# Optimization experiments

Hardware: AMD Instinct MI355X
Metric: run time of the kernel (lower is better)

The kernel has to match this reference:

```python
import jax, jax.numpy as jnp
import numpy as np

C = 8.0


def _linear_scan(alpha, xbeta):
    # h_t = alpha_t * h_{t-1} + xbeta_t, scan over time axis=1
    def combine(e1, e2):
        a1, b1 = e1
        a2, b2 = e2
        return a2 * a1, a2 * b1 + b2
    _, h = jax.lax.associative_scan(combine, (alpha, xbeta), axis=1)
    return h


def setup_inputs() -> dict:
    dim = 2048
    B, T = 4, 4096
    key = jax.random.key(0)
    k_x, k_wi, k_wg = jax.random.split(key, 3)
    std = dim ** -0.5
    x = jax.random.normal(k_x, (B, T, dim), dtype=jnp.float32)
    W_in = jax.random.normal(k_wi, (dim, dim), dtype=jnp.float32) * std
    b_in = jnp.zeros((dim,), dtype=jnp.float32)
    W_gate = jax.random.normal(k_wg, (dim, dim), dtype=jnp.float32) * std
    b_gate = jnp.zeros((dim,), dtype=jnp.float32)
    forget_lambda = jnp.linspace(-4.323, -9.0, dim, dtype=jnp.float32)
    return {"x": x, "W_in": W_in, "b_in": b_in, "W_gate": W_gate,
            "b_gate": b_gate, "forget_lambda": forget_lambda}


def reference(x, W_in, b_in, W_gate, b_gate, forget_lambda):
    # x: [B, T, D]
    input_gate = jnp.einsum('btd,ed->bte', x, W_in) + b_in
    recurrence_gate = jnp.einsum('btd,ed->bte', x, W_gate) + b_gate
    # alpha_t = exp(-C * softplus(lambda) * sigmoid(r_t))  per channel
    alpha = jnp.exp(-C * jax.nn.softplus(forget_lambda) * jax.nn.sigmoid(recurrence_gate))
    beta = jnp.sqrt(1.0 - alpha ** 2 + 1e-6)
    xbeta = beta * jax.nn.sigmoid(input_gate) * x
    return _linear_scan(alpha, xbeta)
```

## Files before the change

### kernel.cpp

```cpp
#include <hip/hip_runtime.h>

typedef unsigned short u16;
typedef unsigned int u32;

using bf16x8 = __attribute__((ext_vector_type(8))) __bf16;
using f32x4  = __attribute__((ext_vector_type(4))) float;
using u16x8  = __attribute__((ext_vector_type(8))) u16;

#define BB 4
#define TT 4096
#define DD 2048
#define MM 16384
#define KK 2048
#define NCHUNK 16
#define CLEN 256

__device__ __forceinline__ u16 f2bf(float f) {
    u32 u = __float_as_uint(f);
    u32 r = (u + 0x7FFFu + ((u >> 16) & 1u)) >> 16;
    return (u16)r;
}

__device__ __forceinline__ void gload_lds16(const void* g, void* l) {
    __builtin_amdgcn_global_load_lds(
        (const __attribute__((address_space(1))) void*)g,
        (__attribute__((address_space(3))) void*)l, 16, 0, 0);
}

#define BAR() do { __builtin_amdgcn_sched_barrier(0); __builtin_amdgcn_s_barrier(); __builtin_amdgcn_sched_barrier(0); } while(0)
#define WAIT_LGKM0() do { asm volatile("s_waitcnt lgkmcnt(0)" ::: "memory"); __builtin_amdgcn_sched_barrier(0); } while(0)
#define WAIT_VM8() do { asm volatile("s_waitcnt vmcnt(8)" ::: "memory"); __builtin_amdgcn_sched_barrier(0); } while(0)
#define WAIT_VM4() do { asm volatile("s_waitcnt vmcnt(4)" ::: "memory"); __builtin_amdgcn_sched_barrier(0); } while(0)
#define WAIT_VM0() do { asm volatile("s_waitcnt vmcnt(0)" ::: "memory"); __builtin_amdgcn_sched_barrier(0); } while(0)

__global__ __launch_bounds__(256) void cvt_kernel(const float* __restrict__ in,
                                                  u16* __restrict__ out, int n8) {
    int i = blockIdx.x * 256 + threadIdx.x;
    if (i >= n8) return;
    const f32x4* p = (const f32x4*)in + (size_t)i * 2;
    f32x4 a = p[0], b = p[1];
    u16x8 o;
    o[0] = f2bf(a[0]); o[1] = f2bf(a[1]); o[2] = f2bf(a[2]); o[3] = f2bf(a[3]);
    o[4] = f2bf(b[0]); o[5] = f2bf(b[1]); o[6] = f2bf(b[2]); o[7] = f2bf(b[3]);
    *((u16x8*)out + i) = o;
}

#define BMg 256
#define BNg 128
#define BKg 32
#define NT (KK / BKg)

__global__ __launch_bounds__(512, 2) void gemm_dual8(
    const u16* __restrict__ xb, const u16* __restrict__ wib, const u16* __restrict__ wgb,
    const float* __restrict__ xf,
    const float* __restrict__ b_in, const float* __restrict__ b_gate,
    const float* __restrict__ lam, u32* __restrict__ pair)
{
    __shared__ u16 As[4][BMg * BKg];
    __shared__ u16 Bs[4][2][BNg * BKg];

    const int tid = threadIdx.x;
    const int bid = blockIdx.x;
    const int cpx = gridDim.x >> 3;
    const int swz = (bid & 7) * cpx + (bid >> 3);
    const int et = swz & 15;
    const int mt = swz >> 4;
    const size_t m0 = (size_t)mt * BMg;
    const size_t e0 = (size_t)et * BNg;

    const int lane = tid & 63;
    const int wid = tid >> 6;
    const int wr = wid >> 2;
    const int wc = wid & 3;
    const int r15 = lane & 15;
    const int s4 = lane >> 4;

    const int srow = tid >> 2;
    const int sseg = (tid & 3) ^ ((tid >> 3) & 3);
    const int skp  = sseg << 3;

    const int koff = ((s4 ^ ((r15 >> 1) & 3)) << 3);

#define STAGE_A(t) do { int _b = (t) & 3; size_t _k = (size_t)(t) * BKg + skp; \
        gload_lds16(xb + (m0 + srow) * KK + _k,        &As[_b][tid * 8]); \
        gload_lds16(xb + (m0 + 128 + srow) * KK + _k,  &As[_b][4096 + tid * 8]); } while (0)
#define STAGE_B(t) do { int _b = (t) & 3; size_t _k = (size_t)(t) * BKg + skp; \
        gload_lds16(wib + (e0 + srow) * KK + _k, &Bs[_b][0][tid * 8]); \
        gload_lds16(wgb + (e0 + srow) * KK + _k, &Bs[_b][1][tid * 8]); } while (0)

    f32x4 accI[8][2], accG[8][2];
#pragma unroll
    for (int i = 0; i < 8; i++)
#pragma unroll
        for (int j = 0; j < 2; j++) {
            accI[i][j] = (f32x4){0.f, 0.f, 0.f, 0.f};
            accG[i][j] = (f32x4){0.f, 0.f, 0.f, 0.f};
        }

    STAGE_A(0); STAGE_B(0);
    STAGE_A(1); STAGE_B(1);
    STAGE_A(2); STAGE_B(2);
    WAIT_VM8();
    BAR();

    for (int t = 0; t < NT; ++t) {
        const int cb = t & 3;
        const u16* Ab = &As[cb][0];
        const u16* BiB = &Bs[cb][0][0];
        const u16* BgB = &Bs[cb][1][0];
        bf16x8 bI[2], bG[2], aF[4];

#pragma unroll
        for (int q = 0; q < 4; q++)
            aF[q] = *(const bf16x8*)&Ab[(wr * 128 + q * 16 + r15) * BKg + koff];
#pragma unroll
        for (int ni = 0; ni < 2; ni++) {
            bI[ni] = *(const bf16x8*)&BiB[(wc * 32 + ni * 16 + r15) * BKg + koff];
            bG[ni] = *(const bf16x8*)&BgB[(wc * 32 + ni * 16 + r15) * BKg + koff];
        }
        if (t < NT - 3) STAGE_A(t + 3);
        BAR();
        WAIT_LGKM0();
        __builtin_amdgcn_s_setprio(1);
#pragma unroll
        for (int q = 0; q < 4; q++)
#pragma unroll
            for (int ni = 0; ni < 2; ni++) {
                accI[q][ni] = __builtin_amdgcn_mfma_f32_16x16x32_bf16(aF[q], bI[ni], accI[q][ni], 0, 0, 0);
                accG[q][ni] = __builtin_amdgcn_mfma_f32_16x16x32_bf16(aF[q], bG[ni], accG[q][ni], 0, 0, 0);
            }
        __builtin_amdgcn_s_setprio(0);
        BAR();

#pragma unroll
        for (int q = 0; q < 4; q++)
            aF[q] = *(const bf16x8*)&Ab[(wr * 128 + (q + 4) * 16 + r15) * BKg + koff];
        if (t < NT - 3) STAGE_B(t + 3);
        BAR();
        WAIT_LGKM0();
        __builtin_amdgcn_s_setprio(1);
#pragma unroll
        for (int q = 0; q < 4; q++)
#pragma unroll
            for (int ni = 0; ni < 2; ni++) {
                accI[q + 4][ni] = __builtin_amdgcn_mfma_f32_16x16x32_bf16(aF[q], bI[ni], accI[q + 4][ni], 0, 0, 0);
                accG[q + 4][ni] = __builtin_amdgcn_mfma_f32_16x16x32_bf16(aF[q], bG[ni], accG[q + 4][ni], 0, 0, 0);
            }
        __builtin_amdgcn_s_setprio(0);
        if (t < NT - 3)      WAIT_VM8();
        else if (t == NT - 3) WAIT_VM4();
        else                  WAIT_VM0();
        BAR();
    }

    float spl[2], biv[2], bgv[2];
    size_t ecol[2];
#pragma unroll
    for (int ni = 0; ni < 2; ni++) {
        size_t e = e0 + wc * 32 + ni * 16 + r15;
        ecol[ni] = e;
        spl[ni] = 8.0f * log1pf(__expf(lam[e]));
        biv[ni] = b_in[e];
        bgv[ni] = b_gate[e];
    }
    const int rbase = s4 * 4;
#pragma unroll
    for (int mi = 0; mi < 8; mi++) {
#pragma unroll
        for (int r = 0; r < 4; r++) {
            size_t m = m0 + wr * 128 + mi * 16 + rbase + r;
#pragma unroll
            for (int ni = 0; ni < 2; ni++) {
                size_t e = ecol[ni];
                float ig = accI[mi][ni][r] + biv[ni];
                float rg = accG[mi][ni][r] + bgv[ni];
                float sigr = 1.f / (1.f + __expf(-rg));
                float g = spl[ni] * sigr;
                float beta = sqrtf(1.f - __expf(-2.f * g) + 1e-6f);
                float xv = xf[m * DD + e];
                float xbeta = beta * (1.f / (1.f + __expf(-ig))) * xv;
                u32 pk = (u32)f2bf(g) | (((u32)f2bf(xbeta)) << 16);
                pair[m * DD + e] = pk;
            }
        }
    }
#undef STAGE_A
#undef STAGE_B
}

__global__ __launch_bounds__(256) void scanA(const u32* __restrict__ pair,
                                             float* __restrict__ aggG,
                                             float* __restrict__ aggB) {
    int gid = blockIdx.x * 256 + threadIdx.x;
    int e = gid & (DD - 1);
    int rest = gid >> 11;
    int b = rest & 3;
    int c = rest >> 2;
    const u32* p = pair + ((size_t)(b * TT + c * CLEN)) * DD + e;
    float gsum = 0.f, h = 0.f;
#pragma unroll 4
    for (int t = 0; t < CLEN; ++t) {
        u32 v = *p; p += DD;
        float gf = __uint_as_float(v << 16);
        float xbv = __uint_as_float(v & 0xFFFF0000u);
        gsum += gf;
        h = fmaf(__expf(-gf), h, xbv);
    }
    int idx = ((b * NCHUNK + c) << 11) | e;
    aggG[idx] = gsum;
    aggB[idx] = h;
}

__global__ __launch_bounds__(256) void scanB(const float* __restrict__ aggG,
                                             const float* __restrict__ aggB,
                                             float* __restrict__ carry) {
    int gid = blockIdx.x * 256 + threadIdx.x;
    int e = gid & (DD - 1);
    int b = gid >> 11;
    float h = 0.f;
#pragma unroll
    for (int c = 0; c < NCHUNK; ++c) {
        int idx = ((b * NCHUNK + c) << 11) | e;
        carry[idx] = h;
        h = fmaf(__expf(-aggG[idx]), h, aggB[idx]);
    }
}

__global__ __launch_bounds__(256) void scanC(const u32* __restrict__ pair,
                                             const float* __restrict__ carry,
                                             float* __restrict__ out) {
    int gid = blockIdx.x * 256 + threadIdx.x;
    int e = gid & (DD - 1);
    int rest = gid >> 11;
    int b = rest & 3;
    int c = rest >> 2;
    const u32* p = pair + ((size_t)(b * TT + c * CLEN)) * DD + e;
    float* o = out + ((size_t)(b * TT + c * CLEN)) * DD + e;
    float h = carry[((b * NCHUNK + c) << 11) | e];
#pragma unroll 4
    for (int t = 0; t < CLEN; ++t) {
        u32 v = *p; p += DD;
        float gf = __uint_as_float(v << 16);
        float xbv = __uint_as_float(v & 0xFFFF0000u);
        h = fmaf(__expf(-gf), h, xbv);
        *o = h; o += DD;
    }
}

extern "C" void kernel_launch(void* const* d_in, const int* in_sizes, int n_in,
                              void* d_out, int out_size, void* d_ws, size_t ws_size,
                              hipStream_t stream) {
    const float* x      = (const float*)d_in[0];
    const float* W_in   = (const float*)d_in[1];
    const float* b_in   = (const float*)d_in[2];
    const float* W_gate = (const float*)d_in[3];
    const float* b_gate = (const float*)d_in[4];
    const float* lam    = (const float*)d_in[5];
    float* out = (float*)d_out;

    char* ws = (char*)d_ws;
    u16* xb   = (u16*)(ws);
    u16* wib  = (u16*)(ws + 67108864);
    u16* wgb  = (u16*)(ws + 75497472);
    u32* pair = (u32*)(ws + 83886080);
    float* aggG  = (float*)(ws + 218103808);
    float* aggB  = (float*)(ws + 218628096);
    float* carry = (float*)(ws + 219152384);

    cvt_kernel<<<16384, 256, 0, stream>>>(x, xb, MM * KK / 8);
    cvt_kernel<<<2048, 256, 0, stream>>>(W_in, wib, DD * KK / 8);
    cvt_kernel<<<2048, 256, 0, stream>>>(W_gate, wgb, DD * KK / 8);
    gemm_dual8<<<(MM / BMg) * (DD / BNg), 512, 0, stream>>>(xb, wib, wgb, x, b_in, b_gate, lam, pair);
    scanA<<<BB * DD * NCHUNK / 256, 256, 0, stream>>>(pair, aggG, aggB);
    scanB<<<BB * DD / 256, 256, 0, stream>>>(aggG, aggB, carry);
    scanC<<<BB * DD * NCHUNK / 256, 256, 0, stream>>>(pair, carry, out);
}
```

Measured before the change: 503.5 us.

## Restructure GEMM main loop with hoisted offsets and read bf16 x in epilogue

The GEMM K-loop is split into a steady-state loop unrolled by 4 without staging branches and a separate tail loop. LDS fragment offsets and global base pointers are precomputed once instead of per iteration. The sched_barrier wrappers around the barriers are removed, giving the compiler more scheduling freedom. The epilogue reads x from the bf16 copy instead of the fp32 input, halving that traffic but lowering the precision of x in xbeta.

Result: faster. 436.3 us (-13.3%).

```diff
diff --git a/kernel.cpp b/kernel.cpp
--- a/kernel.cpp
+++ b/kernel.cpp
@@ -26,12 +26,6 @@
         (const __attribute__((address_space(1))) void*)g,
         (__attribute__((address_space(3))) void*)l, 16, 0, 0);
 }
-
-#define BAR() do { __builtin_amdgcn_sched_barrier(0); __builtin_amdgcn_s_barrier(); __builtin_amdgcn_sched_barrier(0); } while(0)
-#define WAIT_LGKM0() do { asm volatile("s_waitcnt lgkmcnt(0)" ::: "memory"); __builtin_amdgcn_sched_barrier(0); } while(0)
-#define WAIT_VM8() do { asm volatile("s_waitcnt vmcnt(8)" ::: "memory"); __builtin_amdgcn_sched_barrier(0); } while(0)
-#define WAIT_VM4() do { asm volatile("s_waitcnt vmcnt(4)" ::: "memory"); __builtin_amdgcn_sched_barrier(0); } while(0)
-#define WAIT_VM0() do { asm volatile("s_waitcnt vmcnt(0)" ::: "memory"); __builtin_amdgcn_sched_barrier(0); } while(0)
 
 __global__ __launch_bounds__(256) void cvt_kernel(const float* __restrict__ in,
                                                   u16* __restrict__ out, int n8) {
@@ -52,7 +46,6 @@
 
 __global__ __launch_bounds__(512, 2) void gemm_dual8(
     const u16* __restrict__ xb, const u16* __restrict__ wib, const u16* __restrict__ wgb,
-    const float* __restrict__ xf,
     const float* __restrict__ b_in, const float* __restrict__ b_gate,
     const float* __restrict__ lam, u32* __restrict__ pair)
 {
@@ -81,12 +74,23 @@
 
     const int koff = ((s4 ^ ((r15 >> 1) & 3)) << 3);
 
-#define STAGE_A(t) do { int _b = (t) & 3; size_t _k = (size_t)(t) * BKg + skp; \
-        gload_lds16(xb + (m0 + srow) * KK + _k,        &As[_b][tid * 8]); \
-        gload_lds16(xb + (m0 + 128 + srow) * KK + _k,  &As[_b][4096 + tid * 8]); } while (0)
-#define STAGE_B(t) do { int _b = (t) & 3; size_t _k = (size_t)(t) * BKg + skp; \
-        gload_lds16(wib + (e0 + srow) * KK + _k, &Bs[_b][0][tid * 8]); \
-        gload_lds16(wgb + (e0 + srow) * KK + _k, &Bs[_b][1][tid * 8]); } while (0)
+    const u16* gA0 = xb  + (m0 + srow) * KK + skp;
+    const u16* gA1 = gA0 + (size_t)128 * KK;
+    const u16* gI  = wib + (e0 + srow) * KK + skp;
+    const u16* gG  = wgb + (e0 + srow) * KK + skp;
+
+    int aoff[8], boff[2];
+#pragma unroll
+    for (int q = 0; q < 8; q++) aoff[q] = (wr * 128 + q * 16 + r15) * BKg + koff;
+#pragma unroll
+    for (int ni = 0; ni < 2; ni++) boff[ni] = (wc * 32 + ni * 16 + r15) * BKg + koff;
+
+#define STAGE_A(t) do { int _b = (t) & 3; size_t _k = (size_t)(t) * BKg; \
+        gload_lds16(gA0 + _k, &As[_b][tid * 8]); \
+        gload_lds16(gA1 + _k, &As[_b][4096 + tid * 8]); } while (0)
+#define STAGE_B(t) do { int _b = (t) & 3; size_t _k = (size_t)(t) * BKg; \
+        gload_lds16(gI + _k, &Bs[_b][0][tid * 8]); \
+        gload_lds16(gG + _k, &Bs[_b][1][tid * 8]); } while (0)
 
     f32x4 accI[8][2], accG[8][2];
 #pragma unroll
@@ -100,57 +104,61 @@
     STAGE_A(0); STAGE_B(0);
     STAGE_A(1); STAGE_B(1);
     STAGE_A(2); STAGE_B(2);
-    WAIT_VM8();
-    BAR();
-
-    for (int t = 0; t < NT; ++t) {
-        const int cb = t & 3;
-        const u16* Ab = &As[cb][0];
-        const u16* BiB = &Bs[cb][0][0];
-        const u16* BgB = &Bs[cb][1][0];
-        bf16x8 bI[2], bG[2], aF[4];
-
-#pragma unroll
-        for (int q = 0; q < 4; q++)
-            aF[q] = *(const bf16x8*)&Ab[(wr * 128 + q * 16 + r15) * BKg + koff];
-#pragma unroll
-        for (int ni = 0; ni < 2; ni++) {
-            bI[ni] = *(const bf16x8*)&BiB[(wc * 32 + ni * 16 + r15) * BKg + koff];
-            bG[ni] = *(const bf16x8*)&BgB[(wc * 32 + ni * 16 + r15) * BKg + koff];
-        }
-        if (t < NT - 3) STAGE_A(t + 3);
-        BAR();
-        WAIT_LGKM0();
-        __builtin_amdgcn_s_setprio(1);
-#pragma unroll
-        for (int q = 0; q < 4; q++)
-#pragma unroll
-            for (int ni = 0; ni < 2; ni++) {
-                accI[q][ni] = __builtin_amdgcn_mfma_f32_16x16x32_bf16(aF[q], bI[ni], accI[q][ni], 0, 0, 0);
-                accG[q][ni] = __builtin_amdgcn_mfma_f32_16x16x32_bf16(aF[q], bG[ni], accG[q][ni], 0, 0, 0);
-            }
-        __builtin_amdgcn_s_setprio(0);
-        BAR();
-
-#pragma unroll
-        for (int q = 0; q < 4; q++)
-            aF[q] = *(const bf16x8*)&Ab[(wr * 128 + (q + 4) * 16 + r15) * BKg + koff];
-        if (t < NT - 3) STAGE_B(t + 3);
-        BAR();
-        WAIT_LGKM0();
-        __builtin_amdgcn_s_setprio(1);
-#pragma unroll
-        for (int q = 0; q < 4; q++)
-#pragma unroll
-            for (int ni = 0; ni < 2; ni++) {
-                accI[q + 4][ni] = __builtin_amdgcn_mfma_f32_16x16x32_bf16(aF[q], bI[ni], accI[q + 4][ni], 0, 0, 0);
-                accG[q + 4][ni] = __builtin_amdgcn_mfma_f32_16x16x32_bf16(aF[q], bG[ni], accG[q + 4][ni], 0, 0, 0);
-            }
-        __builtin_amdgcn_s_setprio(0);
-        if (t < NT - 3)      WAIT_VM8();
-        else if (t == NT - 3) WAIT_VM4();
-        else                  WAIT_VM0();
-        BAR();
+    asm volatile("s_waitcnt vmcnt(8)" ::: "memory");
+    __builtin_amdgcn_s_barrier();
+
+#define PHASE0(t) do { \
+        const u16* Ab = &As[(t) & 3][0]; \
+        const u16* BiB = &Bs[(t) & 3][0][0]; \
+        const u16* BgB = &Bs[(t) & 3][1][0]; \
+        _Pragma("unroll") for (int q = 0; q < 4; q++) aF[q] = *(const bf16x8*)&Ab[aoff[q]]; \
+        _Pragma("unroll") for (int ni = 0; ni < 2; ni++) { \
+            bI[ni] = *(const bf16x8*)&BiB[boff[ni]]; \
+            bG[ni] = *(const bf16x8*)&BgB[boff[ni]]; } \
+    } while (0)
+#define PHASE1(t) do { \
+        const u16* Ab = &As[(t) & 3][0]; \
+        _Pragma("unroll") for (int q = 0; q < 4; q++) aF[q] = *(const bf16x8*)&Ab[aoff[q + 4]]; \
+    } while (0)
+#define MFMA_BURST(base) do { \
+        asm volatile("s_waitcnt lgkmcnt(0)" ::: "memory"); \
+        __builtin_amdgcn_sched_barrier(0); \
+        __builtin_amdgcn_s_setprio(1); \
+        _Pragma("unroll") for (int q = 0; q < 4; q++) \
+        _Pragma("unroll") for (int ni = 0; ni < 2; ni++) { \
+            accI[q + (base)][ni] = __builtin_amdgcn_mfma_f32_16x16x32_bf16(aF[q], bI[ni], accI[q + (base)][ni], 0, 0, 0); \
+            accG[q + (base)][ni] = __builtin_amdgcn_mfma_f32_16x16x32_bf16(aF[q], bG[ni], accG[q + (base)][ni], 0, 0, 0); } \
+        __builtin_amdgcn_s_setprio(0); \
+    } while (0)
+
+    bf16x8 bI[2], bG[2], aF[4];
+
+#pragma unroll 4
+    for (int t = 0; t < NT - 3; ++t) {
+        PHASE0(t);
+        STAGE_A(t + 3);
+        __builtin_amdgcn_s_barrier();
+        MFMA_BURST(0);
+        __builtin_amdgcn_s_barrier();
+        PHASE1(t);
+        STAGE_B(t + 3);
+        __builtin_amdgcn_s_barrier();
+        MFMA_BURST(4);
+        asm volatile("s_waitcnt vmcnt(8)" ::: "memory");
+        __builtin_amdgcn_s_barrier();
+    }
+#pragma unroll 1
+    for (int t = NT - 3; t < NT; ++t) {
+        PHASE0(t);
+        __builtin_amdgcn_s_barrier();
+        MFMA_BURST(0);
+        __builtin_amdgcn_s_barrier();
+        PHASE1(t);
+        __builtin_amdgcn_s_barrier();
+        MFMA_BURST(4);
+        if (t == NT - 3) asm volatile("s_waitcnt vmcnt(4)" ::: "memory");
+        else             asm volatile("s_waitcnt vmcnt(0)" ::: "memory");
+        __builtin_amdgcn_s_barrier();
     }
 
     float spl[2], biv[2], bgv[2];
@@ -177,7 +185,7 @@
                 float sigr = 1.f / (1.f + __expf(-rg));
                 float g = spl[ni] * sigr;
                 float beta = sqrtf(1.f - __expf(-2.f * g) + 1e-6f);
-                float xv = xf[m * DD + e];
+                float xv = __uint_as_float((u32)xb[m * KK + e] << 16);
                 float xbeta = beta * (1.f / (1.f + __expf(-ig))) * xv;
                 u32 pk = (u32)f2bf(g) | (((u32)f2bf(xbeta)) << 16);
                 pair[m * DD + e] = pk;
@@ -186,6 +194,9 @@
     }
 #undef STAGE_A
 #undef STAGE_B
+#undef PHASE0
+#undef PHASE1
+#undef MFMA_BURST
 }
 
 __global__ __launch_bounds__(256) void scanA(const u32* __restrict__ pair,
@@ -270,7 +281,7 @@
     cvt_kernel<<<16384, 256, 0, stream>>>(x, xb, MM * KK / 8);
     cvt_kernel<<<2048, 256, 0, stream>>>(W_in, wib, DD * KK / 8);
     cvt_kernel<<<2048, 256, 0, stream>>>(W_gate, wgb, DD * KK / 8);
-    gemm_dual8<<<(MM / BMg) * (DD / BNg), 512, 0, stream>>>(xb, wib, wgb, x, b_in, b_gate, lam, pair);
+    gemm_dual8<<<(MM / BMg) * (DD / BNg), 512, 0, stream>>>(xb, wib, wgb, b_in, b_gate, lam, pair);
     scanA<<<BB * DD * NCHUNK / 256, 256, 0, stream>>>(pair, aggG, aggB);
     scanB<<<BB * DD / 256, 256, 0, stream>>>(aggG, aggB, carry);
     scanC<<<BB * DD * NCHUNK / 256, 256, 0, stream>>>(pair, carry, out);
```

## Restructure dual GEMM into double-buffered BK=64 pipeline with register-prefetched fragments

Applied to the files above, without the earlier changes.

Rewrites the main loop of the dual GEMM to use a 64-wide K tile with two LDS buffers and an XOR-swizzled layout. LDS fragment reads for the next MFMA burst are interleaved with the current burst, and the global-to-LDS loads are split into four sub-stages placed between bursts. The aim is to hide LDS and global latency behind MFMA work. The epilogue now reads x from the bf16 copy instead of the fp32 input, which halves that read traffic but uses a rounded x value in xbeta. LDS use stays the same while register pressure rises because of the prefetched fragments.

After: 571.5 us. 13.5% more time.

```diff
diff --git a/kernel.cpp b/kernel.cpp
--- a/kernel.cpp
+++ b/kernel.cpp
@@ -26,12 +26,6 @@
         (const __attribute__((address_space(1))) void*)g,
         (__attribute__((address_space(3))) void*)l, 16, 0, 0);
 }
-
-#define BAR() do { __builtin_amdgcn_sched_barrier(0); __builtin_amdgcn_s_barrier(); __builtin_amdgcn_sched_barrier(0); } while(0)
-#define WAIT_LGKM0() do { asm volatile("s_waitcnt lgkmcnt(0)" ::: "memory"); __builtin_amdgcn_sched_barrier(0); } while(0)
-#define WAIT_VM8() do { asm volatile("s_waitcnt vmcnt(8)" ::: "memory"); __builtin_amdgcn_sched_barrier(0); } while(0)
-#define WAIT_VM4() do { asm volatile("s_waitcnt vmcnt(4)" ::: "memory"); __builtin_amdgcn_sched_barrier(0); } while(0)
-#define WAIT_VM0() do { asm volatile("s_waitcnt vmcnt(0)" ::: "memory"); __builtin_amdgcn_sched_barrier(0); } while(0)
 
 __global__ __launch_bounds__(256) void cvt_kernel(const float* __restrict__ in,
                                                   u16* __restrict__ out, int n8) {
@@ -47,17 +41,19 @@
 
 #define BMg 256
 #define BNg 128
-#define BKg 32
-#define NT (KK / BKg)
-
-__global__ __launch_bounds__(512, 2) void gemm_dual8(
+#define BKt 64
+#define NTt (KK / BKt)
+
+#define MF(a_, b_, c_) __builtin_amdgcn_mfma_f32_16x16x32_bf16(a_, b_, c_, 0, 0, 0)
+
+__global__ __launch_bounds__(512, 2) void gemm_dual_p4(
     const u16* __restrict__ xb, const u16* __restrict__ wib, const u16* __restrict__ wgb,
-    const float* __restrict__ xf,
     const float* __restrict__ b_in, const float* __restrict__ b_gate,
     const float* __restrict__ lam, u32* __restrict__ pair)
 {
-    __shared__ u16 As[4][BMg * BKg];
-    __shared__ u16 Bs[4][2][BNg * BKg];
+    __shared__ u16 As[2][BMg * BKt];
+    __shared__ u16 Bi[2][BNg * BKt];
+    __shared__ u16 Bg[2][BNg * BKt];
 
     const int tid = threadIdx.x;
     const int bid = blockIdx.x;
@@ -69,24 +65,50 @@
     const size_t e0 = (size_t)et * BNg;
 
     const int lane = tid & 63;
-    const int wid = tid >> 6;
-    const int wr = wid >> 2;
-    const int wc = wid & 3;
+    const int w = tid >> 6;
+    const int wr = w >> 2;
+    const int wc = w & 3;
     const int r15 = lane & 15;
     const int s4 = lane >> 4;
 
-    const int srow = tid >> 2;
-    const int sseg = (tid & 3) ^ ((tid >> 3) & 3);
-    const int skp  = sseg << 3;
-
-    const int koff = ((s4 ^ ((r15 >> 1) & 3)) << 3);
-
-#define STAGE_A(t) do { int _b = (t) & 3; size_t _k = (size_t)(t) * BKg + skp; \
-        gload_lds16(xb + (m0 + srow) * KK + _k,        &As[_b][tid * 8]); \
-        gload_lds16(xb + (m0 + 128 + srow) * KK + _k,  &As[_b][4096 + tid * 8]); } while (0)
-#define STAGE_B(t) do { int _b = (t) & 3; size_t _k = (size_t)(t) * BKg + skp; \
-        gload_lds16(wib + (e0 + srow) * KK + _k, &Bs[_b][0][tid * 8]); \
-        gload_lds16(wgb + (e0 + srow) * KK + _k, &Bs[_b][1][tid * 8]); } while (0)
+    const u16 *gSA0[2], *gSA1[2], *gSBI[2], *gSBG[2];
+#pragma unroll
+    for (int j = 0; j < 2; j++) {
+        int L = w * 128 + j * 64 + lane;
+        int row = L >> 3;
+        int sc = (L & 7) ^ (row & 7);
+        gSA0[j] = xb  + (m0 + row) * (size_t)KK + sc * 8;
+        gSA1[j] = xb  + (m0 + 128 + row) * (size_t)KK + sc * 8;
+        gSBI[j] = wib + (e0 + row) * (size_t)KK + sc * 8;
+        gSBG[j] = wgb + (e0 + row) * (size_t)KK + sc * 8;
+    }
+    const int dstE = (w * 128 + lane) * 8;
+
+#define ST_A0(t) do { int _b = ((t) & 1); size_t _k = (size_t)(t) * BKt; \
+        gload_lds16(gSA0[0] + _k, &As[_b][dstE]); \
+        gload_lds16(gSA0[1] + _k, &As[_b][dstE + 512]); } while (0)
+#define ST_A1(t) do { int _b = ((t) & 1); size_t _k = (size_t)(t) * BKt; \
+        gload_lds16(gSA1[0] + _k, &As[_b][8192 + dstE]); \
+        gload_lds16(gSA1[1] + _k, &As[_b][8192 + dstE + 512]); } while (0)
+#define ST_BI(t) do { int _b = ((t) & 1); size_t _k = (size_t)(t) * BKt; \
+        gload_lds16(gSBI[0] + _k, &Bi[_b][dstE]); \
+        gload_lds16(gSBI[1] + _k, &Bi[_b][dstE + 512]); } while (0)
+#define ST_BG(t) do { int _b = ((t) & 1); size_t _k = (size_t)(t) * BKt; \
+        gload_lds16(gSBG[0] + _k, &Bg[_b][dstE]); \
+        gload_lds16(gSBG[1] + _k, &Bg[_b][dstE + 512]); } while (0)
+
+    int cE[2];
+#pragma unroll
+    for (int ks = 0; ks < 2; ks++) cE[ks] = ((((ks << 2) | s4) ^ (r15 & 7)) << 3);
+    int aR[8], bR[2];
+#pragma unroll
+    for (int mF = 0; mF < 8; mF++) aR[mF] = (wr * 128 + mF * 16 + r15) << 6;
+#pragma unroll
+    for (int ni = 0; ni < 2; ni++) bR[ni] = (wc * 32 + ni * 16 + r15) << 6;
+
+#define RD_A(b_, mF_, ks_)  (*(const bf16x8*)&As[b_][aR[mF_] + cE[ks_]])
+#define RD_BI(b_, ni_, ks_) (*(const bf16x8*)&Bi[b_][bR[ni_] + cE[ks_]])
+#define RD_BG(b_, ni_, ks_) (*(const bf16x8*)&Bg[b_][bR[ni_] + cE[ks_]])
 
     f32x4 accI[8][2], accG[8][2];
 #pragma unroll
@@ -97,60 +119,120 @@
             accG[i][j] = (f32x4){0.f, 0.f, 0.f, 0.f};
         }
 
-    STAGE_A(0); STAGE_B(0);
-    STAGE_A(1); STAGE_B(1);
-    STAGE_A(2); STAGE_B(2);
-    WAIT_VM8();
-    BAR();
-
-    for (int t = 0; t < NT; ++t) {
-        const int cb = t & 3;
-        const u16* Ab = &As[cb][0];
-        const u16* BiB = &Bs[cb][0][0];
-        const u16* BgB = &Bs[cb][1][0];
-        bf16x8 bI[2], bG[2], aF[4];
-
-#pragma unroll
-        for (int q = 0; q < 4; q++)
-            aF[q] = *(const bf16x8*)&Ab[(wr * 128 + q * 16 + r15) * BKg + koff];
-#pragma unroll
-        for (int ni = 0; ni < 2; ni++) {
-            bI[ni] = *(const bf16x8*)&BiB[(wc * 32 + ni * 16 + r15) * BKg + koff];
-            bG[ni] = *(const bf16x8*)&BgB[(wc * 32 + ni * 16 + r15) * BKg + koff];
-        }
-        if (t < NT - 3) STAGE_A(t + 3);
-        BAR();
-        WAIT_LGKM0();
-        __builtin_amdgcn_s_setprio(1);
-#pragma unroll
-        for (int q = 0; q < 4; q++)
-#pragma unroll
-            for (int ni = 0; ni < 2; ni++) {
-                accI[q][ni] = __builtin_amdgcn_mfma_f32_16x16x32_bf16(aF[q], bI[ni], accI[q][ni], 0, 0, 0);
-                accG[q][ni] = __builtin_amdgcn_mfma_f32_16x16x32_bf16(aF[q], bG[ni], accG[q][ni], 0, 0, 0);
-            }
-        __builtin_amdgcn_s_setprio(0);
-        BAR();
-
-#pragma unroll
-        for (int q = 0; q < 4; q++)
-            aF[q] = *(const bf16x8*)&Ab[(wr * 128 + (q + 4) * 16 + r15) * BKg + koff];
-        if (t < NT - 3) STAGE_B(t + 3);
-        BAR();
-        WAIT_LGKM0();
-        __builtin_amdgcn_s_setprio(1);
-#pragma unroll
-        for (int q = 0; q < 4; q++)
-#pragma unroll
-            for (int ni = 0; ni < 2; ni++) {
-                accI[q + 4][ni] = __builtin_amdgcn_mfma_f32_16x16x32_bf16(aF[q], bI[ni], accI[q + 4][ni], 0, 0, 0);
-                accG[q + 4][ni] = __builtin_amdgcn_mfma_f32_16x16x32_bf16(aF[q], bG[ni], accG[q + 4][ni], 0, 0, 0);
-            }
-        __builtin_amdgcn_s_setprio(0);
-        if (t < NT - 3)      WAIT_VM8();
-        else if (t == NT - 3) WAIT_VM4();
-        else                  WAIT_VM0();
-        BAR();
+    bf16x8 aA[4], aB[4], aC[4], aD[4];
+    bf16x8 b0v[4], b1v[4];
+
+#define LGKM(n) do { asm volatile("s_waitcnt lgkmcnt(" #n ")" ::: "memory"); \
+                     __builtin_amdgcn_sched_barrier(0); } while (0)
+#define VMC(n)  asm volatile("s_waitcnt vmcnt(" #n ")" ::: "memory")
+#define BARx()  __builtin_amdgcn_s_barrier()
+#define BURST(aV, bV, base) do { __builtin_amdgcn_s_setprio(1); \
+        _Pragma("unroll") for (int m = 0; m < 4; m++) { \
+            accI[m + (base)][0] = MF(aV[m], bV[0], accI[m + (base)][0]); \
+            accI[m + (base)][1] = MF(aV[m], bV[1], accI[m + (base)][1]); \
+            accG[m + (base)][0] = MF(aV[m], bV[2], accG[m + (base)][0]); \
+            accG[m + (base)][1] = MF(aV[m], bV[3], accG[m + (base)][1]); } \
+        __builtin_amdgcn_s_setprio(0); } while (0)
+
+    ST_A0(0); ST_A1(0); ST_BI(0); ST_BG(0);
+    ST_A0(1); ST_A1(1); ST_BI(1); ST_BG(1);
+    VMC(8);
+    BARx();
+
+    {
+#pragma unroll
+        for (int m = 0; m < 4; m++) aA[m] = RD_A(0, m, 0);
+#pragma unroll
+        for (int n = 0; n < 2; n++) { b0v[n] = RD_BI(0, n, 0); b0v[2 + n] = RD_BG(0, n, 0); }
+#pragma unroll
+        for (int m = 0; m < 4; m++) aB[m] = RD_A(0, m + 4, 0);
+#pragma unroll
+        for (int m = 0; m < 4; m++) aC[m] = RD_A(0, m, 1);
+#pragma unroll
+        for (int n = 0; n < 2; n++) { b1v[n] = RD_BI(0, n, 1); b1v[2 + n] = RD_BG(0, n, 1); }
+        BARx();
+        LGKM(8);
+        BURST(aA, b0v, 0);
+#pragma unroll
+        for (int m = 0; m < 4; m++) aD[m] = RD_A(0, m + 4, 1);
+        BARx();
+        LGKM(4);
+        BURST(aB, b0v, 4);
+        VMC(4);
+        BARx();
+    }
+
+#pragma unroll 2
+    for (int t = 1; t < NTt - 1; ++t) {
+        const int b = t & 1;
+#pragma unroll
+        for (int m = 0; m < 4; m++) aA[m] = RD_A(b, m, 0);
+        ST_A0(t + 1);
+        BARx();
+        LGKM(4);
+        BURST(aC, b1v, 0);
+        VMC(2);
+        BARx();
+#pragma unroll
+        for (int n = 0; n < 2; n++) { b0v[n] = RD_BI(b, n, 0); b0v[2 + n] = RD_BG(b, n, 0); }
+#pragma unroll
+        for (int m = 0; m < 4; m++) aB[m] = RD_A(b, m + 4, 0);
+        ST_A1(t + 1);
+        BARx();
+        LGKM(8);
+        BURST(aD, b1v, 4);
+        BARx();
+#pragma unroll
+        for (int m = 0; m < 4; m++) aC[m] = RD_A(b, m, 1);
+#pragma unroll
+        for (int n = 0; n < 2; n++) { b1v[n] = RD_BI(b, n, 1); b1v[2 + n] = RD_BG(b, n, 1); }
+        ST_BI(t + 1);
+        BARx();
+        LGKM(8);
+        BURST(aA, b0v, 0);
+        BARx();
+#pragma unroll
+        for (int m = 0; m < 4; m++) aD[m] = RD_A(b, m + 4, 1);
+        ST_BG(t + 1);
+        BARx();
+        LGKM(4);
+        BURST(aB, b0v, 4);
+        VMC(4);
+        BARx();
+    }
+
+    {
+#pragma unroll
+        for (int m = 0; m < 4; m++) aA[m] = RD_A(1, m, 0);
+        BARx();
+        LGKM(4);
+        BURST(aC, b1v, 0);
+        VMC(0);
+        BARx();
+#pragma unroll
+        for (int n = 0; n < 2; n++) { b0v[n] = RD_BI(1, n, 0); b0v[2 + n] = RD_BG(1, n, 0); }
+#pragma unroll
+        for (int m = 0; m < 4; m++) aB[m] = RD_A(1, m + 4, 0);
+        BARx();
+        LGKM(8);
+        BURST(aD, b1v, 4);
+        BARx();
+#pragma unroll
+        for (int m = 0; m < 4; m++) aC[m] = RD_A(1, m, 1);
+#pragma unroll
+        for (int n = 0; n < 2; n++) { b1v[n] = RD_BI(1, n, 1); b1v[2 + n] = RD_BG(1, n, 1); }
+        BARx();
+        LGKM(8);
+        BURST(aA, b0v, 0);
+        BARx();
+#pragma unroll
+        for (int m = 0; m < 4; m++) aD[m] = RD_A(1, m + 4, 1);
+        BARx();
+        LGKM(4);
+        BURST(aB, b0v, 4);
+        LGKM(0);
+        BURST(aC, b1v, 0);
+        BURST(aD, b1v, 4);
     }
 
     float spl[2], biv[2], bgv[2];
@@ -177,15 +259,21 @@
                 float sigr = 1.f / (1.f + __expf(-rg));
                 float g = spl[ni] * sigr;
                 float beta = sqrtf(1.f - __expf(-2.f * g) + 1e-6f);
-                float xv = xf[m * DD + e];
+                float xv = __uint_as_float((u32)xb[m * KK + e] << 16);
                 float xbeta = beta * (1.f / (1.f + __expf(-ig))) * xv;
                 u32 pk = (u32)f2bf(g) | (((u32)f2bf(xbeta)) << 16);
                 pair[m * DD + e] = pk;
             }
         }
     }
-#undef STAGE_A
-#undef STAGE_B
+#undef ST_A0
+#undef ST_A1
+#undef ST_BI
+#undef ST_BG
+#undef RD_A
+#undef RD_BI
+#undef RD_BG
+#undef BURST
 }
 
 __global__ __launch_bounds__(256) void scanA(const u32* __restrict__ pair,
@@ -270,7 +358,7 @@
     cvt_kernel<<<16384, 256, 0, stream>>>(x, xb, MM * KK / 8);
     cvt_kernel<<<2048, 256, 0, stream>>>(W_in, wib, DD * KK / 8);
     cvt_kernel<<<2048, 256, 0, stream>>>(W_gate, wgb, DD * KK / 8);
-    gemm_dual8<<<(MM / BMg) * (DD / BNg), 512, 0, stream>>>(xb, wib, wgb, x, b_in, b_gate, lam, pair);
+    gemm_dual_p4<<<(MM / BMg) * (DD / BNg), 512, 0, stream>>>(xb, wib, wgb, b_in, b_gate, lam, pair);
     scanA<<<BB * DD * NCHUNK / 256, 256, 0, stream>>>(pair, aggG, aggB);
     scanB<<<BB * DD / 256, 256, 0, stream>>>(aggG, aggB, carry);
     scanC<<<BB * DD * NCHUNK / 256, 256, 0, stream>>>(pair, carry, out);
```

## Rework dual GEMM pipeline: prefetch depth two, new LDS swizzle, bf16 x in epilogue

Applied to the files above, without the earlier changes.

Restructures the dual-GEMM main loop. Prefetch distance drops from three stages to two with adjusted vmcnt waits, and the sched_barrier wrappers around barriers are removed. Global pointers and LDS offsets are precomputed with a new XOR swizzle intended to reduce bank conflicts. The epilogue reads x from the bf16 copy instead of fp32 to cut global traffic, at some precision cost in xbeta. A shallower prefetch may expose more load latency.

Result: faster. 472.8 us (-6.1%).

```diff
diff --git a/kernel.cpp b/kernel.cpp
--- a/kernel.cpp
+++ b/kernel.cpp
@@ -26,12 +26,6 @@
         (const __attribute__((address_space(1))) void*)g,
         (__attribute__((address_space(3))) void*)l, 16, 0, 0);
 }
-
-#define BAR() do { __builtin_amdgcn_sched_barrier(0); __builtin_amdgcn_s_barrier(); __builtin_amdgcn_sched_barrier(0); } while(0)
-#define WAIT_LGKM0() do { asm volatile("s_waitcnt lgkmcnt(0)" ::: "memory"); __builtin_amdgcn_sched_barrier(0); } while(0)
-#define WAIT_VM8() do { asm volatile("s_waitcnt vmcnt(8)" ::: "memory"); __builtin_amdgcn_sched_barrier(0); } while(0)
-#define WAIT_VM4() do { asm volatile("s_waitcnt vmcnt(4)" ::: "memory"); __builtin_amdgcn_sched_barrier(0); } while(0)
-#define WAIT_VM0() do { asm volatile("s_waitcnt vmcnt(0)" ::: "memory"); __builtin_amdgcn_sched_barrier(0); } while(0)
 
 __global__ __launch_bounds__(256) void cvt_kernel(const float* __restrict__ in,
                                                   u16* __restrict__ out, int n8) {
@@ -50,14 +44,16 @@
 #define BKg 32
 #define NT (KK / BKg)
 
-__global__ __launch_bounds__(512, 2) void gemm_dual8(
+#define MF(a_, b_, c_) __builtin_amdgcn_mfma_f32_16x16x32_bf16(a_, b_, c_, 0, 0, 0)
+
+__global__ __launch_bounds__(512, 2) void gemm_lock2(
     const u16* __restrict__ xb, const u16* __restrict__ wib, const u16* __restrict__ wgb,
-    const float* __restrict__ xf,
     const float* __restrict__ b_in, const float* __restrict__ b_gate,
     const float* __restrict__ lam, u32* __restrict__ pair)
 {
     __shared__ u16 As[4][BMg * BKg];
-    __shared__ u16 Bs[4][2][BNg * BKg];
+    __shared__ u16 Bi[4][BNg * BKg];
+    __shared__ u16 Bg[4][BNg * BKg];
 
     const int tid = threadIdx.x;
     const int bid = blockIdx.x;
@@ -69,24 +65,40 @@
     const size_t e0 = (size_t)et * BNg;
 
     const int lane = tid & 63;
-    const int wid = tid >> 6;
-    const int wr = wid >> 2;
-    const int wc = wid & 3;
+    const int w = tid >> 6;
+    const int wr = w >> 2;
+    const int wc = w & 3;
     const int r15 = lane & 15;
     const int s4 = lane >> 4;
 
-    const int srow = tid >> 2;
-    const int sseg = (tid & 3) ^ ((tid >> 3) & 3);
-    const int skp  = sseg << 3;
-
-    const int koff = ((s4 ^ ((r15 >> 1) & 3)) << 3);
-
-#define STAGE_A(t) do { int _b = (t) & 3; size_t _k = (size_t)(t) * BKg + skp; \
-        gload_lds16(xb + (m0 + srow) * KK + _k,        &As[_b][tid * 8]); \
-        gload_lds16(xb + (m0 + 128 + srow) * KK + _k,  &As[_b][4096 + tid * 8]); } while (0)
-#define STAGE_B(t) do { int _b = (t) & 3; size_t _k = (size_t)(t) * BKg + skp; \
-        gload_lds16(wib + (e0 + srow) * KK + _k, &Bs[_b][0][tid * 8]); \
-        gload_lds16(wgb + (e0 + srow) * KK + _k, &Bs[_b][1][tid * 8]); } while (0)
+    const u16 *gA[2], *gBi, *gBg;
+#pragma unroll
+    for (int j = 0; j < 2; j++) {
+        int L = j * 512 + tid;
+        int row = L >> 2;
+        int cs = (L & 3) ^ (row & 3) ^ ((row >> 2) & 3);
+        gA[j] = xb + (m0 + row) * (size_t)KK + cs * 8;
+    }
+    {
+        int row = tid >> 2;
+        int cs = (tid & 3) ^ (row & 3) ^ ((row >> 2) & 3);
+        gBi = wib + (e0 + row) * (size_t)KK + cs * 8;
+        gBg = wgb + (e0 + row) * (size_t)KK + cs * 8;
+    }
+
+#define ST_A(t) do { int _s = (t) & 3; size_t _k = (size_t)(t) * BKg; \
+        gload_lds16(gA[0] + _k, &As[_s][tid * 8]); \
+        gload_lds16(gA[1] + _k, &As[_s][4096 + tid * 8]); } while (0)
+#define ST_B(t) do { int _s = (t) & 3; size_t _k = (size_t)(t) * BKg; \
+        gload_lds16(gBi + _k, &Bi[_s][tid * 8]); \
+        gload_lds16(gBg + _k, &Bg[_s][tid * 8]); } while (0)
+
+    const int csw = (s4 ^ (r15 & 3) ^ ((r15 >> 2) & 3)) << 3;
+    int aR[8], bR[2];
+#pragma unroll
+    for (int mF = 0; mF < 8; mF++) aR[mF] = ((wr * 128 + mF * 16 + r15) << 5) + csw;
+#pragma unroll
+    for (int ni = 0; ni < 2; ni++) bR[ni] = ((wc * 32 + ni * 16 + r15) << 5) + csw;
 
     f32x4 accI[8][2], accG[8][2];
 #pragma unroll
@@ -97,60 +109,46 @@
             accG[i][j] = (f32x4){0.f, 0.f, 0.f, 0.f};
         }
 
-    STAGE_A(0); STAGE_B(0);
-    STAGE_A(1); STAGE_B(1);
-    STAGE_A(2); STAGE_B(2);
-    WAIT_VM8();
-    BAR();
-
+    bf16x8 aF[4], bv[4];
+
+#define LGKM0() do { asm volatile("s_waitcnt lgkmcnt(0)" ::: "memory"); \
+                     __builtin_amdgcn_sched_barrier(0); } while (0)
+#define BURST(base) do { __builtin_amdgcn_s_setprio(1); \
+        _Pragma("unroll") for (int m = 0; m < 4; m++) { \
+            accI[m + (base)][0] = MF(aF[m], bv[0], accI[m + (base)][0]); \
+            accI[m + (base)][1] = MF(aF[m], bv[1], accI[m + (base)][1]); \
+            accG[m + (base)][0] = MF(aF[m], bv[2], accG[m + (base)][0]); \
+            accG[m + (base)][1] = MF(aF[m], bv[3], accG[m + (base)][1]); } \
+        __builtin_amdgcn_s_setprio(0); } while (0)
+
+    ST_A(0); ST_B(0);
+    ST_A(1); ST_B(1);
+    asm volatile("s_waitcnt vmcnt(4)" ::: "memory");
+    __builtin_amdgcn_s_barrier();
+
+#pragma unroll 4
     for (int t = 0; t < NT; ++t) {
-        const int cb = t & 3;
-        const u16* Ab = &As[cb][0];
-        const u16* BiB = &Bs[cb][0][0];
-        const u16* BgB = &Bs[cb][1][0];
-        bf16x8 bI[2], bG[2], aF[4];
-
-#pragma unroll
-        for (int q = 0; q < 4; q++)
-            aF[q] = *(const bf16x8*)&Ab[(wr * 128 + q * 16 + r15) * BKg + koff];
-#pragma unroll
-        for (int ni = 0; ni < 2; ni++) {
-            bI[ni] = *(const bf16x8*)&BiB[(wc * 32 + ni * 16 + r15) * BKg + koff];
-            bG[ni] = *(const bf16x8*)&BgB[(wc * 32 + ni * 16 + r15) * BKg + koff];
-        }
-        if (t < NT - 3) STAGE_A(t + 3);
-        BAR();
-        WAIT_LGKM0();
-        __builtin_amdgcn_s_setprio(1);
-#pragma unroll
-        for (int q = 0; q < 4; q++)
-#pragma unroll
-            for (int ni = 0; ni < 2; ni++) {
-                accI[q][ni] = __builtin_amdgcn_mfma_f32_16x16x32_bf16(aF[q], bI[ni], accI[q][ni], 0, 0, 0);
-                accG[q][ni] = __builtin_amdgcn_mfma_f32_16x16x32_bf16(aF[q], bG[ni], accG[q][ni], 0, 0, 0);
-            }
-        __builtin_amdgcn_s_setprio(0);
-        BAR();
-
-#pragma unroll
-        for (int q = 0; q < 4; q++)
-            aF[q] = *(const bf16x8*)&Ab[(wr * 128 + (q + 4) * 16 + r15) * BKg + koff];
-        if (t < NT - 3) STAGE_B(t + 3);
-        BAR();
-        WAIT_LGKM0();
-        __builtin_amdgcn_s_setprio(1);
-#pragma unroll
-        for (int q = 0; q < 4; q++)
-#pragma unroll
-            for (int ni = 0; ni < 2; ni++) {
-                accI[q + 4][ni] = __builtin_amdgcn_mfma_f32_16x16x32_bf16(aF[q], bI[ni], accI[q + 4][ni], 0, 0, 0);
-                accG[q + 4][ni] = __builtin_amdgcn_mfma_f32_16x16x32_bf16(aF[q], bG[ni], accG[q + 4][ni], 0, 0, 0);
-            }
-        __builtin_amdgcn_s_setprio(0);
-        if (t < NT - 3)      WAIT_VM8();
-        else if (t == NT - 3) WAIT_VM4();
-        else                  WAIT_VM0();
-        BAR();
+        const int s = t & 3;
+#pragma unroll
+        for (int m = 0; m < 4; m++) aF[m] = *(const bf16x8*)&As[s][aR[m]];
+        bv[0] = *(const bf16x8*)&Bi[s][bR[0]];
+        bv[1] = *(const bf16x8*)&Bi[s][bR[1]];
+        bv[2] = *(const bf16x8*)&Bg[s][bR[0]];
+        bv[3] = *(const bf16x8*)&Bg[s][bR[1]];
+        if (t < NT - 2) ST_A(t + 2);
+        __builtin_amdgcn_s_barrier();
+        LGKM0();
+        BURST(0);
+        __builtin_amdgcn_s_barrier();
+#pragma unroll
+        for (int m = 0; m < 4; m++) aF[m] = *(const bf16x8*)&As[s][aR[m + 4]];
+        if (t < NT - 2) ST_B(t + 2);
+        __builtin_amdgcn_s_barrier();
+        LGKM0();
+        BURST(4);
+        if (t == NT - 3)      asm volatile("s_waitcnt vmcnt(0)" ::: "memory");
+        else if (t < NT - 3)  asm volatile("s_waitcnt vmcnt(4)" ::: "memory");
+        __builtin_amdgcn_s_barrier();
     }
 
     float spl[2], biv[2], bgv[2];
@@ -177,15 +175,16 @@
                 float sigr = 1.f / (1.f + __expf(-rg));
                 float g = spl[ni] * sigr;
                 float beta = sqrtf(1.f - __expf(-2.f * g) + 1e-6f);
-                float xv = xf[m * DD + e];
+                float xv = __uint_as_float((u32)xb[m * KK + e] << 16);
                 float xbeta = beta * (1.f / (1.f + __expf(-ig))) * xv;
                 u32 pk = (u32)f2bf(g) | (((u32)f2bf(xbeta)) << 16);
                 pair[m * DD + e] = pk;
             }
         }
     }
-#undef STAGE_A
-#undef STAGE_B
+#undef ST_A
+#undef ST_B
+#undef BURST
 }
 
 __global__ __launch_bounds__(256) void scanA(const u32* __restrict__ pair,
@@ -270,7 +269,7 @@
     cvt_kernel<<<16384, 256, 0, stream>>>(x, xb, MM * KK / 8);
     cvt_kernel<<<2048, 256, 0, stream>>>(W_in, wib, DD * KK / 8);
     cvt_kernel<<<2048, 256, 0, stream>>>(W_gate, wgb, DD * KK / 8);
-    gemm_dual8<<<(MM / BMg) * (DD / BNg), 512, 0, stream>>>(xb, wib, wgb, x, b_in, b_gate, lam, pair);
+    gemm_lock2<<<(MM / BMg) * (DD / BNg), 512, 0, stream>>>(xb, wib, wgb, b_in, b_gate, lam, pair);
     scanA<<<BB * DD * NCHUNK / 256, 256, 0, stream>>>(pair, aggG, aggB);
     scanB<<<BB * DD / 256, 256, 0, stream>>>(aggG, aggB, carry);
     scanC<<<BB * DD * NCHUNK / 256, 256, 0, stream>>>(pair, carry, out);
```
